# Optimization experiments

Measured on AMD Instinct MI355X. Metric: run time of the kernel, lower is better.

## Reference

```python
import math
import jax, jax.numpy as jnp
from jax import lax
import numpy as np

B, M, L = 256, 21, 512
P, S, D = 16, 8, 256
NL, EXP, H, LAM = 3, 2, 96, 0.01
T = (L - P) // S + 1  # 63 patches
HID = D * EXP


def _pos_enc():
    pe = np.zeros((T, D), np.float32)
    pos = np.arange(T, dtype=np.float32)[:, None]
    div = np.exp(np.arange(0, D, 2, dtype=np.float32) * (-math.log(10000.0) / D))
    pe[:, 0::2] = np.sin(pos * div)
    pe[:, 1::2] = np.cos(pos * div)
    return jnp.asarray(pe)


def _clin(zr, zi, Wr, Wi, br, bi):
    # faithful to torch: bias br added to both terms of yr (cancels), bi added twice in yi
    yr = (zr @ Wr.T + br) - (zi @ Wi.T + br)
    yi = (zr @ Wi.T + bi) + (zi @ Wr.T + bi)
    return yr, yi


def _softshrink(zr, zi):
    mag = jnp.sqrt(zr * zr + zi * zi)
    scale = jnp.maximum(mag - LAM, 0.0) / (mag + 1e-8) * (mag > LAM).astype(zr.dtype)
    return zr * scale, zi * scale


def _layernorm(x, g, b):
    mu = jnp.mean(x, -1, keepdims=True)
    var = jnp.mean((x - mu) ** 2, -1, keepdims=True)
    return (x - mu) / jnp.sqrt(var + 1e-5) * g + b


def _block(x, p):
    (Tw, Tb, Gew, Geb, Gpw, Gpb,
     H1Wr, H1Wi, H1br, H1bi, H2Wr, H2Wi, H2br, H2bi, lng, lnb) = p
    g = jax.nn.gelu(x @ Gew.T + Geb, approximate=False) @ Gpw.T + Gpb
    zf = jnp.fft.rfft(x, axis=1)  # FFT along time/patch axis T
    zr, zi = zf.real, zf.imag
    zr, zi = _clin(zr, zi, H1Wr, H1Wi, H1br, H1bi)
    zr, zi = _softshrink(zr, zi)
    zr, zi = _clin(zr, zi, H2Wr, H2Wi, H2br, H2bi)
    pt = jnp.fft.irfft(lax.complex(zr, zi), n=x.shape[1], axis=1)
    out = (g * pt) @ Tw.T + Tb
    return _layernorm(out + x, lng, lnb)


def _forward(x, conv_w, conv_b, tp, sp, gate_w, gate_b, proj_w, proj_b):
    # per-instance, per-variable norm over time (biased std, eps on std)
    mean = jnp.mean(x, -1, keepdims=True)
    std = jnp.sqrt(jnp.mean((x - mean) ** 2, -1, keepdims=True))
    xn = (x - mean) / (std + 1e-5)
    patches = lax.conv_general_dilated(xn, conv_w, (S,), 'VALID',
                                       dimension_numbers=('NCH', 'OIH', 'NCH'))
    patches = patches + conv_b[None, :, None]
    h = patches.transpose(0, 2, 1) + _pos_enc()[None]  # (B, T, D)
    t = h
    s = h
    for i in range(NL):
        t = _block(t, tuple(a[i] for a in tp))
        s = _block(s, tuple(a[i] for a in sp))
    gate = jax.nn.sigmoid(t @ gate_w.T + gate_b)
    feat = gate * t + (1.0 - gate) * s
    out = feat.reshape(feat.shape[0], -1) @ proj_w.T + proj_b
    y = out.reshape(-1, M, H) * (std + 1e-5) + mean
    return y


def setup_inputs() -> dict:
    key = jax.random.key(0)
    ks = iter(jax.random.split(key, 64))

    def nrm(shape, scale):
        return jax.random.normal(next(ks), shape, jnp.float32) * scale

    inp = {'x': nrm((B, M, L), 1.0)}
    inp['conv_w'] = nrm((D, M, P), 1.0 / math.sqrt(M * P))
    inp['conv_b'] = jnp.zeros((D,), jnp.float32)

    def layer_params(prefix):
        d = {}
        d[prefix + 'Tw'] = nrm((NL, D, D), 1.0 / math.sqrt(D))
        d[prefix + 'Tb'] = jnp.zeros((NL, D), jnp.float32)
        d[prefix + 'Gew'] = nrm((NL, HID, D), 1.0 / math.sqrt(D))
        d[prefix + 'Geb'] = jnp.zeros((NL, HID), jnp.float32)
        d[prefix + 'Gpw'] = nrm((NL, D, HID), 1.0 / math.sqrt(HID))
        d[prefix + 'Gpb'] = jnp.zeros((NL, D), jnp.float32)
        for hname in ('H1', 'H2'):
            d[prefix + hname + 'Wr'] = nrm((NL, D, D), 1.0 / math.sqrt(D))
            d[prefix + hname + 'Wi'] = nrm((NL, D, D), 1.0 / math.sqrt(D))
            d[prefix + hname + 'br'] = jnp.zeros((NL, D), jnp.float32)
            d[prefix + hname + 'bi'] = jnp.zeros((NL, D), jnp.float32)
        d[prefix + 'lng'] = jnp.ones((NL, D), jnp.float32)
        d[prefix + 'lnb'] = jnp.zeros((NL, D), jnp.float32)
        return d

    inp.update(layer_params('t_'))
    inp.update(layer_params('s_'))
    inp['gate_w'] = nrm((1, D), 1.0 / math.sqrt(D))
    inp['gate_b'] = jnp.zeros((1,), jnp.float32)
    inp['proj_w'] = nrm((M * H, T * D), 1.0 / math.sqrt(T * D))
    inp['proj_b'] = jnp.zeros((M * H,), jnp.float32)
    return inp


def reference(x, conv_w, conv_b,
              t_Tw, t_Tb, t_Gew, t_Geb, t_Gpw, t_Gpb,
              t_H1Wr, t_H1Wi, t_H1br, t_H1bi, t_H2Wr, t_H2Wi, t_H2br, t_H2bi, t_lng, t_lnb,
              s_Tw, s_Tb, s_Gew, s_Geb, s_Gpw, s_Gpb,
              s_H1Wr, s_H1Wi, s_H1br, s_H1bi, s_H2Wr, s_H2Wi, s_H2br, s_H2bi, s_lng, s_lnb,
              gate_w, gate_b, proj_w, proj_b):
    tp = (t_Tw, t_Tb, t_Gew, t_Geb, t_Gpw, t_Gpb,
          t_H1Wr, t_H1Wi, t_H1br, t_H1bi, t_H2Wr, t_H2Wi, t_H2br, t_H2bi, t_lng, t_lnb)
    sp = (s_Tw, s_Tb, s_Gew, s_Geb, s_Gpw, s_Gpb,
          s_H1Wr, s_H1Wi, s_H1br, s_H1bi, s_H2Wr, s_H2Wi, s_H2br, s_H2bi, s_lng, s_lnb)
    return _forward(x, conv_w, conv_b, tp, sp, gate_w, gate_b, proj_w, proj_b)
```

## Files before the change

kernel.cpp:

```cpp
#include <hip/hip_runtime.h>
#include <cstddef>
#include <cstdint>

#define B_    256
#define M_    21
#define L_    512
#define D_    256
#define T_    63
#define F_    32
#define NT_   16128
#define HID_  512
#define KCP_  352
#define H_    96
#define LAM_  0.01f
#define PZ_   14

typedef __attribute__((ext_vector_type(8))) short short8;
typedef __attribute__((ext_vector_type(4))) float f32x4;
typedef unsigned int u32;
typedef const u32 __attribute__((address_space(1)))* gas1_t;
typedef u32 __attribute__((address_space(3)))* las3_t;

__device__ __forceinline__ void async_copy16(const void* g, void* l) {
  __builtin_amdgcn_global_load_lds((gas1_t)g, (las3_t)(uintptr_t)l, 16, 0, 0);
}
__device__ __forceinline__ unsigned short f2bf(float x) {
  unsigned u = __float_as_uint(x);
  return (unsigned short)((u + 0x7FFF + ((u >> 16) & 1)) >> 16);
}
__device__ __forceinline__ float bf2f(unsigned short u) {
  return __uint_as_float(((unsigned)u) << 16);
}
__device__ __forceinline__ float gelu_exact(float v) {
  return 0.5f * v * (1.0f + erff(v * 0.70710678118654752f));
}
__device__ __forceinline__ float block_sum256(float v, float* red4) {
  #pragma unroll
  for (int off = 32; off > 0; off >>= 1) v += __shfl_down(v, off, 64);
  if ((threadIdx.x & 63) == 0) red4[threadIdx.x >> 6] = v;
  __syncthreads();
  float r = red4[0] + red4[1] + red4[2] + red4[3];
  __syncthreads();
  return r;
}
__device__ __forceinline__ float wave_sum(float v) {
  #pragma unroll
  for (int off = 1; off < 64; off <<= 1) v += __shfl_xor(v, off, 64);
  return v;
}

struct CvtEnt { const float* src; unsigned short* dst; int rows, scol, dcol, blk0; };
struct CvtArgs { CvtEnt e[19]; int nent; };
__global__ __launch_bounds__(256) void wprep_kernel(CvtArgs a) {
  int blk = blockIdx.x, e = 0;
  while (e + 1 < a.nent && a.e[e + 1].blk0 <= blk) ++e;
  CvtEnt en = a.e[e];
  int idx = (blk - en.blk0) * 256 + threadIdx.x;
  int total = en.rows * en.dcol;
  if (idx >= total) return;
  int r = idx / en.dcol, c = idx - r * en.dcol;
  float v = (c < en.scol) ? en.src[(size_t)r * en.scol + c] : 0.f;
  en.dst[idx] = f2bf(v);
}

struct CatArgs { const float* wr[12]; const float* wi[12]; };
__global__ __launch_bounds__(256) void wcat_kernel(CatArgs a, unsigned short* dst) {
  int e = blockIdx.x >> 10;
  int idx = ((blockIdx.x & 1023) << 8) + threadIdx.x;
  int r = idx >> 9, c = idx & 511;
  int cp = r >> 1, p = r & 1, d = c >> 1, q = c & 1;
  const float* wr = a.wr[e];
  const float* wi = a.wi[e];
  float v;
  if (p == 0) v = (q == 0) ? wr[cp * 256 + d] : -wi[cp * 256 + d];
  else        v = (q == 0) ? wi[cp * 256 + d] :  wr[cp * 256 + d];
  dst[(size_t)e * 262144 + idx] = f2bf(v);
}

template <int ACT, int OUTBF, int BIASM, int KSTEPS, int CVTA, int CVTW,
          int SHRINK, int MULPT, int SPLITK, int BK>
__global__ __launch_bounds__(256) void mm_kernel(
    const void* __restrict__ Av,
    const unsigned short* __restrict__ W0, const unsigned short* __restrict__ W1,
    const float* __restrict__ Wf,
    const float* __restrict__ b0, const float* __restrict__ b1,
    const unsigned short* __restrict__ ptb,
    void* __restrict__ Cv,
    const int K, const int Dout, const int ksteps_rt, const int yhalf, const int prow) {
  constexpr int NP = BK / 32;
  __shared__ __align__(16) unsigned short As[NP * 128 * 32];
  __shared__ __align__(16) unsigned short Bs[NP * 128 * 32];
  const int ksteps = KSTEPS ? KSTEPS : ksteps_rt;
  const int tid = threadIdx.x, w = tid >> 6, lane = tid & 63;
  const int quad = lane >> 4, r16 = lane & 15;
  const int kst = SPLITK ? (int)blockIdx.z * ksteps * BK : 0;
  const int tower = ((int)blockIdx.y >= yhalf) ? 1 : 0;
  const unsigned short* Wb = tower ? W1 : W0;
  const float* bias = tower ? b1 : b0;

  const unsigned short* Ab = (const unsigned short*)Av;
  const float* Af = (const float*)Av;
  const unsigned short* gA = nullptr;
  unsigned short* lA = As + (w * 32) * 32;
  if (!CVTA) gA = Ab + (size_t)(blockIdx.y * 128 + w * 32 + (lane >> 2)) * K
                     + kst + (lane & 3) * 8;
  const unsigned short* gB = nullptr;
  unsigned short* lB = Bs + (w * 32) * 32;
  if (!CVTW) gB = Wb + (size_t)(blockIdx.x * 128 + w * 32 + (lane >> 2)) * K
                     + kst + (lane & 3) * 8;
  const int crow = tid >> 3;
  const int ck4  = (tid & 7) << 2;

  f32x4 acc[4][4];
  #pragma unroll
  for (int i = 0; i < 4; ++i)
    #pragma unroll
    for (int j = 0; j < 4; ++j)
      #pragma unroll
      for (int r = 0; r < 4; ++r) acc[i][j][r] = 0.f;

  for (int ks = 0; ks < ksteps; ++ks) {
    if (!CVTA) {
      #pragma unroll
      for (int p = 0; p < NP; ++p) {
        async_copy16(gA + p * 32, lA + p * 4096);
        async_copy16(gA + (size_t)16 * K + p * 32, lA + p * 4096 + 16 * 32);
      }
      gA += BK;
    } else {
      #pragma unroll
      for (int p = 0; p < NP; ++p)
        #pragma unroll
        for (int rr = 0; rr < 4; ++rr) {
          int row128 = crow + 32 * rr;
          const float* asrc = Af + (size_t)((int)blockIdx.y * 128 + row128) * K
                                 + ks * BK + p * 32 + ck4;
          float4 v = *reinterpret_cast<const float4*>(asrc);
          ushort4 o; o.x = f2bf(v.x); o.y = f2bf(v.y); o.z = f2bf(v.z); o.w = f2bf(v.w);
          *reinterpret_cast<ushort4*>(As + p * 4096 + row128 * 32 + ck4) = o;
        }
    }
    if (!CVTW) {
      #pragma unroll
      for (int p = 0; p < NP; ++p) {
        async_copy16(gB + p * 32, lB + p * 4096);
        async_copy16(gB + (size_t)16 * K + p * 32, lB + p * 4096 + 16 * 32);
      }
      gB += BK;
    } else {
      #pragma unroll
      for (int p = 0; p < NP; ++p)
        #pragma unroll
        for (int rr = 0; rr < 4; ++rr) {
          int row128 = crow + 32 * rr;
          int wrow = blockIdx.x * 128 + row128;
          if (wrow >= Dout) wrow = Dout - 1;
          const float* wsrc = Wf + (size_t)wrow * K + kst + ks * BK + p * 32 + ck4;
          float4 v = *reinterpret_cast<const float4*>(wsrc);
          ushort4 o; o.x = f2bf(v.x); o.y = f2bf(v.y); o.z = f2bf(v.z); o.w = f2bf(v.w);
          *reinterpret_cast<ushort4*>(Bs + p * 4096 + row128 * 32 + ck4) = o;
        }
    }
    __syncthreads();
    #pragma unroll
    for (int p = 0; p < NP; ++p) {
      const unsigned short* pa = As + p * 4096 + (64 * (w >> 1) + r16) * 32 + quad * 8;
      const unsigned short* pb = Bs + p * 4096 + (64 * (w & 1) + r16) * 32 + quad * 8;
      short8 af[4], bfv[4];
      #pragma unroll
      for (int i = 0; i < 4; ++i) af[i] = *reinterpret_cast<const short8*>(pa + i * 512);
      #pragma unroll
      for (int j = 0; j < 4; ++j) bfv[j] = *reinterpret_cast<const short8*>(pb + j * 512);
      #pragma unroll
      for (int i = 0; i < 4; ++i)
        #pragma unroll
        for (int j = 0; j < 4; ++j)
          acc[i][j] = __builtin_amdgcn_mfma_f32_16x16x32_bf16(af[i], bfv[j], acc[i][j], 0, 0, 0);
    }
    __syncthreads();
  }

  float* Cf = (float*)Cv;
  unsigned short* Cb = (unsigned short*)Cv;
  if (SPLITK) Cf += (size_t)blockIdx.z * prow * Dout;
  const int colb = blockIdx.x * 128 + 64 * (w & 1) + r16;
  const int rowb = blockIdx.y * 128 + 64 * (w >> 1) + quad * 4;
  #pragma unroll
  for (int j = 0; j < 4; ++j) {
    int col = colb + 16 * j;
    float bv = 0.f;
    if (BIASM == 0) bv = bias[col];
    else if (BIASM == 1) bv = (col & 1) ? 2.0f * bias[col >> 1] : 0.f;
    bool colok = (BIASM != 2) || (col < Dout);
    #pragma unroll
    for (int i = 0; i < 4; ++i) {
      #pragma unroll
      for (int r = 0; r < 4; ++r) {
        int row = rowb + 16 * i + r;
        float v = acc[i][j][r] + bv;
        if (ACT == 1) v = gelu_exact(v);
        if (SHRINK) {
          float o = __shfl_xor(v, 1, 64);
          float mag = sqrtf(v * v + o * o);
          float s = (mag > LAM_) ? (mag - LAM_) / (mag + 1e-8f) : 0.f;
          v *= s;
        }
        if (MULPT) v *= bf2f(ptb[(size_t)row * Dout + col]);
        if (colok) {
          if (OUTBF) Cb[(size_t)row * Dout + col] = f2bf(v);
          else       Cf[(size_t)row * Dout + col] = v;
        }
      }
    }
  }
}

__global__ __launch_bounds__(256) void norm_kernel(const float* __restrict__ x,
    float* __restrict__ xn, float* __restrict__ meanb, float* __restrict__ stdb) {
  __shared__ float red[4];
  int bm = blockIdx.x;
  const float* xr = x + (size_t)bm * L_;
  float v0 = xr[threadIdx.x], v1 = xr[threadIdx.x + 256];
  float mu = block_sum256(v0 + v1, red) * (1.0f / L_);
  float d0 = v0 - mu, d1 = v1 - mu;
  float sd = sqrtf(block_sum256(d0 * d0 + d1 * d1, red) * (1.0f / L_));
  float inv = 1.0f / (sd + 1e-5f);
  float* xo = xn + (size_t)bm * L_;
  xo[threadIdx.x] = d0 * inv;
  xo[threadIdx.x + 256] = d1 * inv;
  if (threadIdx.x == 0) { meanb[bm] = mu; stdb[bm] = sd; }
}

__global__ __launch_bounds__(256) void im2col_kernel(const float* __restrict__ xn,
                                                     unsigned short* __restrict__ im) {
  int row = blockIdx.x;
  int b = row / T_, t = row - b * T_;
  const float* xb = xn + (size_t)b * M_ * L_ + t * 8;
  unsigned short* o = im + (size_t)row * KCP_;
  for (int i = threadIdx.x; i < KCP_; i += 256) {
    float v = 0.f;
    if (i < 336) { int m = i >> 4, p = i & 15; v = xb[m * L_ + p]; }
    o[i] = f2bf(v);
  }
}

__global__ __launch_bounds__(256) void add_pe_kernel(const float* __restrict__ g0,
                                                     float* __restrict__ x32) {
  int row = blockIdx.x, d = threadIdx.x;
  int t = row % T_;
  size_t idx = (size_t)row * D_ + d;
  float freq = expf((float)(d & ~1) * (-9.210340371976184f / 256.0f));
  float ang = (float)t * freq;
  float pe = (d & 1) ? cosf(ang) : sinf(ang);
  float h = g0[idx] + pe;
  x32[idx] = h;
  x32[idx + (size_t)NT_ * D_] = h;
}

__global__ __launch_bounds__(256) void dft_kernel(const float* __restrict__ X,
                                                  unsigned short* __restrict__ Zcat) {
  __shared__ float2 tw[T_ * F_];
  int bt = blockIdx.x, d = threadIdx.x;
  for (int i = threadIdx.x; i < T_ * F_; i += 256) {
    int t = i >> 5, f = i & 31;
    int k = (f * t) % T_;
    float sn, cs;
    sincosf((6.283185307179586f / 63.0f) * (float)k, &sn, &cs);
    tw[i] = make_float2(cs, -sn);
  }
  __syncthreads();
  const float* xb = X + (size_t)bt * T_ * D_ + d;
  float ar[F_], ai[F_];
  #pragma unroll
  for (int f = 0; f < F_; ++f) { ar[f] = 0.f; ai[f] = 0.f; }
  for (int t = 0; t < T_; ++t) {
    float v = xb[(size_t)t * D_];
    const float2* w = &tw[t * F_];
    #pragma unroll
    for (int f = 0; f < F_; ++f) {
      float2 c = w[f];
      ar[f] = fmaf(v, c.x, ar[f]);
      ai[f] = fmaf(v, c.y, ai[f]);
    }
  }
  u32* z = reinterpret_cast<u32*>(Zcat + (size_t)bt * F_ * 512);
  #pragma unroll
  for (int f = 0; f < F_; ++f)
    z[f * 256 + d] = (u32)f2bf(ar[f]) | ((u32)f2bf(ai[f]) << 16);
}

__global__ __launch_bounds__(256) void irfft_kernel(const unsigned short* __restrict__ Y,
                                                    unsigned short* __restrict__ ptb) {
  __shared__ float2 tw[T_ * 31];
  int bt = blockIdx.x, d = threadIdx.x;
  for (int i = threadIdx.x; i < T_ * 31; i += 256) {
    int t = i / 31, f = i - t * 31 + 1;
    int k = (f * t) % T_;
    float sn, cs;
    sincosf((6.283185307179586f / 63.0f) * (float)k, &sn, &cs);
    tw[i] = make_float2(cs * (2.0f / 63.0f), -sn * (2.0f / 63.0f));
  }
  __syncthreads();
  const unsigned short* yb = Y + (size_t)bt * F_ * 512 + 2 * d;
  float y0 = bf2f(yb[0]) * (1.0f / 63.0f);
  float yr[31], yi[31];
  #pragma unroll
  for (int f = 1; f < F_; ++f) {
    u32 p = *reinterpret_cast<const u32*>(yb + (size_t)f * 512);
    yr[f - 1] = bf2f((unsigned short)(p & 0xffff));
    yi[f - 1] = bf2f((unsigned short)(p >> 16));
  }
  unsigned short* po = ptb + (size_t)bt * T_ * D_ + d;
  for (int t = 0; t < T_; ++t) {
    const float2* w = &tw[t * 31];
    float acc0 = y0, acc1 = 0.f;
    #pragma unroll
    for (int f = 0; f < 31; f += 2) {
      float2 c = w[f];
      acc0 = fmaf(yr[f], c.x, fmaf(yi[f], c.y, acc0));
      if (f + 1 < 31) {
        float2 c1 = w[f + 1];
        acc1 = fmaf(yr[f + 1], c1.x, fmaf(yi[f + 1], c1.y, acc1));
      }
    }
    po[(size_t)t * D_] = f2bf(acc0 + acc1);
  }
}

__global__ __launch_bounds__(256) void ln_kernel(const float* __restrict__ outb,
    float* __restrict__ x, const float* __restrict__ g0, const float* __restrict__ b0,
    const float* __restrict__ g1, const float* __restrict__ b1, int yhalf) {
  int row = blockIdx.x * 4 + (threadIdx.x >> 6);
  int lane = threadIdx.x & 63;
  const float* g = (row >= yhalf) ? g1 : g0;
  const float* b = (row >= yhalf) ? b1 : b0;
  size_t base = (size_t)row * D_ + lane * 4;
  float4 ov = *reinterpret_cast<const float4*>(outb + base);
  float4 xv = *reinterpret_cast<const float4*>(x + base);
  float v0 = ov.x + xv.x, v1 = ov.y + xv.y, v2 = ov.z + xv.z, v3 = ov.w + xv.w;
  float mu = wave_sum(v0 + v1 + v2 + v3) * (1.0f / D_);
  v0 -= mu; v1 -= mu; v2 -= mu; v3 -= mu;
  float var = wave_sum(v0 * v0 + v1 * v1 + v2 * v2 + v3 * v3) * (1.0f / D_);
  float is = rsqrtf(var + 1e-5f);
  float4 gv = *reinterpret_cast<const float4*>(g + lane * 4);
  float4 bv = *reinterpret_cast<const float4*>(b + lane * 4);
  float4 o;
  o.x = v0 * is * gv.x + bv.x;
  o.y = v1 * is * gv.y + bv.y;
  o.z = v2 * is * gv.z + bv.z;
  o.w = v3 * is * gv.w + bv.w;
  *reinterpret_cast<float4*>(x + base) = o;
}

__global__ __launch_bounds__(256) void gate_feat_kernel(const float* __restrict__ x32,
    const float* __restrict__ gw, const float* __restrict__ gb,
    unsigned short* __restrict__ featbf) {
  int row = blockIdx.x * 4 + (threadIdx.x >> 6);
  int lane = threadIdx.x & 63;
  size_t base = (size_t)row * D_ + lane * 4;
  float4 tv = *reinterpret_cast<const float4*>(x32 + base);
  float4 sv = *reinterpret_cast<const float4*>(x32 + base + (size_t)NT_ * D_);
  float4 gv = *reinterpret_cast<const float4*>(gw + lane * 4);
  float dot = wave_sum(tv.x * gv.x + tv.y * gv.y + tv.z * gv.z + tv.w * gv.w) + gb[0];
  float gate = 1.0f / (1.0f + expf(-dot));
  ushort4 o;
  o.x = f2bf(gate * tv.x + (1.0f - gate) * sv.x);
  o.y = f2bf(gate * tv.y + (1.0f - gate) * sv.y);
  o.z = f2bf(gate * tv.z + (1.0f - gate) * sv.z);
  o.w = f2bf(gate * tv.w + (1.0f - gate) * sv.w);
  *reinterpret_cast<ushort4*>(featbf + base) = o;
}

__global__ __launch_bounds__(256) void final_kernel(const float* __restrict__ part,
    const float* __restrict__ pb, const float* __restrict__ stdb,
    const float* __restrict__ meanb, float* __restrict__ y) {
  int i = blockIdx.x * 256 + threadIdx.x;
  float acc = 0.f;
  #pragma unroll
  for (int z = 0; z < PZ_; ++z) acc += part[(size_t)z * 516096 + i];
  int b = i / 2016;
  int col = i - b * 2016;
  int m = col / H_;
  float sc = stdb[b * M_ + m] + 1e-5f;
  y[i] = (acc + pb[col]) * sc + meanb[b * M_ + m];
}

extern "C" void kernel_launch(void* const* d_in, const int* in_sizes, int n_in,
                              void* d_out, int out_size, void* d_ws, size_t ws_size,
                              hipStream_t stream) {
  const float* x      = (const float*)d_in[0];
  const float* conv_w = (const float*)d_in[1];
  const float* conv_b = (const float*)d_in[2];
  const float* tP[16];
  const float* sP[16];
  for (int i = 0; i < 16; ++i) tP[i] = (const float*)d_in[3 + i];
  for (int i = 0; i < 16; ++i) sP[i] = (const float*)d_in[19 + i];
  const float* gate_w = (const float*)d_in[35];
  const float* gate_b = (const float*)d_in[36];
  const float* proj_w = (const float*)d_in[37];
  const float* proj_b = (const float*)d_in[38];
  float* out = (float*)d_out;

  float* ws    = (float*)d_ws;
  float* x32   = ws;
  unsigned short* wb = (unsigned short*)(x32 + 8257536);
  float* meanb = x32 + 8257536 + 2600960;
  float* stdb  = meanb + 5376;
  float* R1    = stdb + 5376 + 16;
  float* R2    = R1 + 8388608;

  unsigned short* im2colB = (unsigned short*)R1;
  unsigned short* Zcat    = (unsigned short*)R1;
  unsigned short* Ycat1   = (unsigned short*)(R1 + 4194304);
  unsigned short* ptb     = (unsigned short*)(R1 + 4194304);
  unsigned short* gp      = (unsigned short*)R1;
  unsigned short* featbf  = (unsigned short*)R1;

  float* xn     = R2;
  float* g0buf  = R2;
  unsigned short* Ycat2b = (unsigned short*)R2;
  unsigned short* hidB = (unsigned short*)R2;
  float* outb   = R2;
  float* part   = R2;

  unsigned short* convW = wb;
  unsigned short* sets  = wb + 90112;
  unsigned short* catW  = wb + 90112 + 1966080;

  CvtArgs ca; int blk0 = 0, ne = 0;
  auto add_ent = [&](const float* s, unsigned short* d, int rows, int scol, int dcol) {
    ca.e[ne].src = s; ca.e[ne].dst = d; ca.e[ne].rows = rows;
    ca.e[ne].scol = scol; ca.e[ne].dcol = dcol; ca.e[ne].blk0 = blk0;
    blk0 += (rows * dcol + 255) / 256; ++ne;
  };
  add_ent(conv_w, convW, 256, 336, 352);
  for (int tw = 0; tw < 2; ++tw) {
    const float** Pp = tw ? (const float**)sP : (const float**)tP;
    for (int l = 0; l < 3; ++l) {
      unsigned short* sb = sets + (size_t)(tw * 3 + l) * 327680;
      add_ent(Pp[2] + (size_t)l * 131072, sb,          512, 256, 256);
      add_ent(Pp[4] + (size_t)l * 131072, sb + 131072, 256, 512, 512);
      add_ent(Pp[0] + (size_t)l * 65536,  sb + 262144, 256, 256, 256);
    }
  }
  ca.nent = ne;
  wprep_kernel<<<blk0, 256, 0, stream>>>(ca);

  CatArgs cat;
  for (int tw = 0; tw < 2; ++tw) {
    const float** Pp = tw ? (const float**)sP : (const float**)tP;
    for (int l = 0; l < 3; ++l) {
      int e0 = (tw * 3 + l) * 2;
      cat.wr[e0]     = Pp[6]  + (size_t)l * 65536;
      cat.wi[e0]     = Pp[7]  + (size_t)l * 65536;
      cat.wr[e0 + 1] = Pp[10] + (size_t)l * 65536;
      cat.wi[e0 + 1] = Pp[11] + (size_t)l * 65536;
    }
  }
  wcat_kernel<<<12 * 1024, 256, 0, stream>>>(cat, catW);

  norm_kernel<<<B_ * M_, 256, 0, stream>>>(x, xn, meanb, stdb);
  im2col_kernel<<<NT_, 256, 0, stream>>>(xn, im2colB);
  mm_kernel<0, 0, 0, 11, 0, 0, 0, 0, 0, 32><<<dim3(2, 126), 256, 0, stream>>>(
      im2colB, convW, convW, nullptr, conv_b, conv_b, nullptr, g0buf,
      KCP_, 256, 0, 1 << 30, 0);
  add_pe_kernel<<<NT_, 256, 0, stream>>>(g0buf, x32);

  for (int l = 0; l < 3; ++l) {
    unsigned short* st0 = sets + (size_t)l * 327680;
    unsigned short* st1 = sets + (size_t)(3 + l) * 327680;
    unsigned short* c1t0 = catW + (size_t)((0 + l) * 2) * 262144;
    unsigned short* c2t0 = c1t0 + 262144;
    unsigned short* c1t1 = catW + (size_t)((3 + l) * 2) * 262144;
    unsigned short* c2t1 = c1t1 + 262144;

    dft_kernel<<<2 * B_, 256, 0, stream>>>(x32, Zcat);
    mm_kernel<0, 1, 1, 8, 0, 0, 1, 0, 0, 64><<<dim3(4, 128), 256, 0, stream>>>(
        Zcat, c1t0, c1t1, nullptr, tP[9] + (size_t)l * D_, sP[9] + (size_t)l * D_,
        nullptr, Ycat1, 512, 512, 0, 64, 0);
    mm_kernel<0, 1, 1, 8, 0, 0, 0, 0, 0, 64><<<dim3(4, 128), 256, 0, stream>>>(
        Ycat1, c2t0, c2t1, nullptr, tP[13] + (size_t)l * D_, sP[13] + (size_t)l * D_,
        nullptr, Ycat2b, 512, 512, 0, 64, 0);
    irfft_kernel<<<2 * B_, 256, 0, stream>>>(Ycat2b, ptb);
    mm_kernel<1, 1, 0, 4, 1, 0, 0, 0, 0, 64><<<dim3(4, 252), 256, 0, stream>>>(
        x32, st0, st1, nullptr, tP[3] + (size_t)l * HID_, sP[3] + (size_t)l * HID_,
        nullptr, hidB, 256, 512, 0, 126, 0);
    mm_kernel<0, 1, 0, 8, 0, 0, 0, 1, 0, 64><<<dim3(2, 252), 256, 0, stream>>>(
        hidB, st0 + 131072, st1 + 131072, nullptr,
        tP[5] + (size_t)l * D_, sP[5] + (size_t)l * D_, ptb, gp, 512, 256, 0, 126, 0);
    mm_kernel<0, 0, 0, 4, 0, 0, 0, 0, 0, 64><<<dim3(2, 252), 256, 0, stream>>>(
        gp, st0 + 262144, st1 + 262144, nullptr,
        tP[1] + (size_t)l * D_, sP[1] + (size_t)l * D_, nullptr, outb, 256, 256, 0, 126, 0);
    ln_kernel<<<2 * NT_ / 4, 256, 0, stream>>>(outb, x32,
        tP[14] + (size_t)l * D_, tP[15] + (size_t)l * D_,
        sP[14] + (size_t)l * D_, sP[15] + (size_t)l * D_, NT_);
  }

  gate_feat_kernel<<<NT_ / 4, 256, 0, stream>>>(x32, gate_w, gate_b, featbf);
  mm_kernel<0, 0, 2, 0, 0, 1, 0, 0, 1, 32><<<dim3(16, 2, PZ_), 256, 0, stream>>>(
      featbf, nullptr, nullptr, proj_w, nullptr, nullptr, nullptr, part,
      NT_, 2016, 504 / PZ_, 1 << 30, 256);
  final_kernel<<<2016, 256, 0, stream>>>(part, proj_b, stdb, meanb, out);
}
```

Measured before the change: 1.022 ms.

## Halve GEMM row tile via RT template, prefetch fp32 operands into registers

Adds an RT template parameter so every GEMM uses 64-row A tiles instead of 128, doubling grid size in y for all matmul launches to raise occupancy and block count. Fp32-converted A and W tiles are now loaded into registers one k-step ahead, overlapping global loads with MFMA work. The split-K projection is retiled to 16 partitions with a clamped tail. Smaller tiles lower per-block reuse of the B tile and increase total weight traffic.

```diff
diff --git a/kernel.cpp b/kernel.cpp
--- a/kernel.cpp
+++ b/kernel.cpp
@@ -13,7 +13,7 @@
 #define KCP_  352
 #define H_    96
 #define LAM_  0.01f
-#define PZ_   14
+#define PZ_   16
 
 typedef __attribute__((ext_vector_type(8))) short short8;
 typedef __attribute__((ext_vector_type(4))) float f32x4;
@@ -78,7 +78,7 @@
 }
 
 template <int ACT, int OUTBF, int BIASM, int KSTEPS, int CVTA, int CVTW,
-          int SHRINK, int MULPT, int SPLITK, int BK>
+          int SHRINK, int MULPT, int SPLITK, int BK, int RT>
 __global__ __launch_bounds__(256) void mm_kernel(
     const void* __restrict__ Av,
     const unsigned short* __restrict__ W0, const unsigned short* __restrict__ W1,
@@ -86,14 +86,18 @@
     const float* __restrict__ b0, const float* __restrict__ b1,
     const unsigned short* __restrict__ ptb,
     void* __restrict__ Cv,
-    const int K, const int Dout, const int ksteps_rt, const int yhalf, const int prow) {
+    const int K, const int Dout, const int ksteps_rt, const int yhalf,
+    const int prow, const int totk) {
   constexpr int NP = BK / 32;
-  __shared__ __align__(16) unsigned short As[NP * 128 * 32];
+  constexpr int RWS = 32 * RT;
+  __shared__ __align__(16) unsigned short As[NP * RWS * 32];
   __shared__ __align__(16) unsigned short Bs[NP * 128 * 32];
-  const int ksteps = KSTEPS ? KSTEPS : ksteps_rt;
   const int tid = threadIdx.x, w = tid >> 6, lane = tid & 63;
   const int quad = lane >> 4, r16 = lane & 15;
-  const int kst = SPLITK ? (int)blockIdx.z * ksteps * BK : 0;
+  int nks = KSTEPS ? KSTEPS : ksteps_rt;
+  const int ksbeg = SPLITK ? (int)blockIdx.z * nks : 0;
+  if (SPLITK) { int rem = totk - ksbeg; if (nks > rem) nks = rem; }
+  const int kst = ksbeg * BK;
   const int tower = ((int)blockIdx.y >= yhalf) ? 1 : 0;
   const unsigned short* Wb = tower ? W1 : W0;
   const float* bias = tower ? b1 : b0;
@@ -101,43 +105,66 @@
   const unsigned short* Ab = (const unsigned short*)Av;
   const float* Af = (const float*)Av;
   const unsigned short* gA = nullptr;
-  unsigned short* lA = As + (w * 32) * 32;
-  if (!CVTA) gA = Ab + (size_t)(blockIdx.y * 128 + w * 32 + (lane >> 2)) * K
+  unsigned short* lA = As + (w * 8 * RT) * 32;
+  if (!CVTA) gA = Ab + (size_t)((int)blockIdx.y * RWS + w * 8 * RT + (lane >> 2)) * K
                      + kst + (lane & 3) * 8;
   const unsigned short* gB = nullptr;
   unsigned short* lB = Bs + (w * 32) * 32;
-  if (!CVTW) gB = Wb + (size_t)(blockIdx.x * 128 + w * 32 + (lane >> 2)) * K
+  if (!CVTW) gB = Wb + (size_t)((int)blockIdx.x * 128 + w * 32 + (lane >> 2)) * K
                      + kst + (lane & 3) * 8;
   const int crow = tid >> 3;
   const int ck4  = (tid & 7) << 2;
 
-  f32x4 acc[4][4];
-  #pragma unroll
-  for (int i = 0; i < 4; ++i)
+  float4 areg[NP][RT];
+  float4 wreg[NP][4];
+  auto loadA = [&](int ksi) {
+    #pragma unroll
+    for (int p = 0; p < NP; ++p)
+      #pragma unroll
+      for (int rr = 0; rr < RT; ++rr)
+        areg[p][rr] = *reinterpret_cast<const float4*>(
+            Af + (size_t)((int)blockIdx.y * RWS + crow + 32 * rr) * K
+               + kst + ksi * BK + p * 32 + ck4);
+  };
+  auto loadW = [&](int ksi) {
+    #pragma unroll
+    for (int p = 0; p < NP; ++p)
+      #pragma unroll
+      for (int rr = 0; rr < 4; ++rr) {
+        int wrow = (int)blockIdx.x * 128 + crow + 32 * rr;
+        if (wrow >= Dout) wrow = Dout - 1;
+        wreg[p][rr] = *reinterpret_cast<const float4*>(
+            Wf + (size_t)wrow * K + kst + ksi * BK + p * 32 + ck4);
+      }
+  };
+  if (CVTA) loadA(0);
+  if (CVTW) loadW(0);
+
+  f32x4 acc[RT][4];
+  #pragma unroll
+  for (int i = 0; i < RT; ++i)
     #pragma unroll
     for (int j = 0; j < 4; ++j)
       #pragma unroll
       for (int r = 0; r < 4; ++r) acc[i][j][r] = 0.f;
 
-  for (int ks = 0; ks < ksteps; ++ks) {
+  for (int ks = 0; ks < nks; ++ks) {
     if (!CVTA) {
       #pragma unroll
-      for (int p = 0; p < NP; ++p) {
-        async_copy16(gA + p * 32, lA + p * 4096);
-        async_copy16(gA + (size_t)16 * K + p * 32, lA + p * 4096 + 16 * 32);
-      }
+      for (int p = 0; p < NP; ++p)
+        #pragma unroll
+        for (int c = 0; c < RT / 2; ++c)
+          async_copy16(gA + (size_t)(c * 16) * K + p * 32,
+                       lA + p * (RWS * 32) + c * 16 * 32);
       gA += BK;
     } else {
       #pragma unroll
       for (int p = 0; p < NP; ++p)
         #pragma unroll
-        for (int rr = 0; rr < 4; ++rr) {
-          int row128 = crow + 32 * rr;
-          const float* asrc = Af + (size_t)((int)blockIdx.y * 128 + row128) * K
-                                 + ks * BK + p * 32 + ck4;
-          float4 v = *reinterpret_cast<const float4*>(asrc);
+        for (int rr = 0; rr < RT; ++rr) {
+          float4 v = areg[p][rr];
           ushort4 o; o.x = f2bf(v.x); o.y = f2bf(v.y); o.z = f2bf(v.z); o.w = f2bf(v.w);
-          *reinterpret_cast<ushort4*>(As + p * 4096 + row128 * 32 + ck4) = o;
+          *reinterpret_cast<ushort4*>(As + p * (RWS * 32) + (crow + 32 * rr) * 32 + ck4) = o;
         }
     }
     if (!CVTW) {
@@ -152,27 +179,25 @@
       for (int p = 0; p < NP; ++p)
         #pragma unroll
         for (int rr = 0; rr < 4; ++rr) {
-          int row128 = crow + 32 * rr;
-          int wrow = blockIdx.x * 128 + row128;
-          if (wrow >= Dout) wrow = Dout - 1;
-          const float* wsrc = Wf + (size_t)wrow * K + kst + ks * BK + p * 32 + ck4;
-          float4 v = *reinterpret_cast<const float4*>(wsrc);
+          float4 v = wreg[p][rr];
           ushort4 o; o.x = f2bf(v.x); o.y = f2bf(v.y); o.z = f2bf(v.z); o.w = f2bf(v.w);
-          *reinterpret_cast<ushort4*>(Bs + p * 4096 + row128 * 32 + ck4) = o;
+          *reinterpret_cast<ushort4*>(Bs + p * 4096 + (crow + 32 * rr) * 32 + ck4) = o;
         }
     }
     __syncthreads();
+    if (CVTA && ks + 1 < nks) loadA(ks + 1);
+    if (CVTW && ks + 1 < nks) loadW(ks + 1);
     #pragma unroll
     for (int p = 0; p < NP; ++p) {
-      const unsigned short* pa = As + p * 4096 + (64 * (w >> 1) + r16) * 32 + quad * 8;
+      const unsigned short* pa = As + p * (RWS * 32) + ((w >> 1) * 16 * RT + r16) * 32 + quad * 8;
       const unsigned short* pb = Bs + p * 4096 + (64 * (w & 1) + r16) * 32 + quad * 8;
-      short8 af[4], bfv[4];
-      #pragma unroll
-      for (int i = 0; i < 4; ++i) af[i] = *reinterpret_cast<const short8*>(pa + i * 512);
+      short8 af[RT], bfv[4];
+      #pragma unroll
+      for (int i = 0; i < RT; ++i) af[i] = *reinterpret_cast<const short8*>(pa + i * 512);
       #pragma unroll
       for (int j = 0; j < 4; ++j) bfv[j] = *reinterpret_cast<const short8*>(pb + j * 512);
       #pragma unroll
-      for (int i = 0; i < 4; ++i)
+      for (int i = 0; i < RT; ++i)
         #pragma unroll
         for (int j = 0; j < 4; ++j)
           acc[i][j] = __builtin_amdgcn_mfma_f32_16x16x32_bf16(af[i], bfv[j], acc[i][j], 0, 0, 0);
@@ -183,8 +208,8 @@
   float* Cf = (float*)Cv;
   unsigned short* Cb = (unsigned short*)Cv;
   if (SPLITK) Cf += (size_t)blockIdx.z * prow * Dout;
-  const int colb = blockIdx.x * 128 + 64 * (w & 1) + r16;
-  const int rowb = blockIdx.y * 128 + 64 * (w >> 1) + quad * 4;
+  const int colb = (int)blockIdx.x * 128 + 64 * (w & 1) + r16;
+  const int rowb = (int)blockIdx.y * RWS + 16 * RT * (w >> 1) + quad * 4;
   #pragma unroll
   for (int j = 0; j < 4; ++j) {
     int col = colb + 16 * j;
@@ -193,7 +218,7 @@
     else if (BIASM == 1) bv = (col & 1) ? 2.0f * bias[col >> 1] : 0.f;
     bool colok = (BIASM != 2) || (col < Dout);
     #pragma unroll
-    for (int i = 0; i < 4; ++i) {
+    for (int i = 0; i < RT; ++i) {
       #pragma unroll
       for (int r = 0; r < 4; ++r) {
         int row = rowb + 16 * i + r;
@@ -461,9 +486,9 @@
 
   norm_kernel<<<B_ * M_, 256, 0, stream>>>(x, xn, meanb, stdb);
   im2col_kernel<<<NT_, 256, 0, stream>>>(xn, im2colB);
-  mm_kernel<0, 0, 0, 11, 0, 0, 0, 0, 0, 32><<<dim3(2, 126), 256, 0, stream>>>(
+  mm_kernel<0, 0, 0, 11, 0, 0, 0, 0, 0, 32, 2><<<dim3(2, 252), 256, 0, stream>>>(
       im2colB, convW, convW, nullptr, conv_b, conv_b, nullptr, g0buf,
-      KCP_, 256, 0, 1 << 30, 0);
+      KCP_, 256, 0, 1 << 30, 0, 0);
   add_pe_kernel<<<NT_, 256, 0, stream>>>(g0buf, x32);
 
   for (int l = 0; l < 3; ++l) {
@@ -475,30 +500,30 @@
     unsigned short* c2t1 = c1t1 + 262144;
 
     dft_kernel<<<2 * B_, 256, 0, stream>>>(x32, Zcat);
-    mm_kernel<0, 1, 1, 8, 0, 0, 1, 0, 0, 64><<<dim3(4, 128), 256, 0, stream>>>(
+    mm_kernel<0, 1, 1, 8, 0, 0, 1, 0, 0, 64, 2><<<dim3(4, 256), 256, 0, stream>>>(
         Zcat, c1t0, c1t1, nullptr, tP[9] + (size_t)l * D_, sP[9] + (size_t)l * D_,
-        nullptr, Ycat1, 512, 512, 0, 64, 0);
-    mm_kernel<0, 1, 1, 8, 0, 0, 0, 0, 0, 64><<<dim3(4, 128), 256, 0, stream>>>(
+        nullptr, Ycat1, 512, 512, 0, 128, 0, 0);
+    mm_kernel<0, 1, 1, 8, 0, 0, 0, 0, 0, 64, 2><<<dim3(4, 256), 256, 0, stream>>>(
         Ycat1, c2t0, c2t1, nullptr, tP[13] + (size_t)l * D_, sP[13] + (size_t)l * D_,
-        nullptr, Ycat2b, 512, 512, 0, 64, 0);
+        nullptr, Ycat2b, 512, 512, 0, 128, 0, 0);
     irfft_kernel<<<2 * B_, 256, 0, stream>>>(Ycat2b, ptb);
-    mm_kernel<1, 1, 0, 4, 1, 0, 0, 0, 0, 64><<<dim3(4, 252), 256, 0, stream>>>(
+    mm_kernel<1, 1, 0, 4, 1, 0, 0, 0, 0, 64, 2><<<dim3(4, 504), 256, 0, stream>>>(
         x32, st0, st1, nullptr, tP[3] + (size_t)l * HID_, sP[3] + (size_t)l * HID_,
-        nullptr, hidB, 256, 512, 0, 126, 0);
-    mm_kernel<0, 1, 0, 8, 0, 0, 0, 1, 0, 64><<<dim3(2, 252), 256, 0, stream>>>(
+        nullptr, hidB, 256, 512, 0, 252, 0, 0);
+    mm_kernel<0, 1, 0, 8, 0, 0, 0, 1, 0, 64, 2><<<dim3(2, 504), 256, 0, stream>>>(
         hidB, st0 + 131072, st1 + 131072, nullptr,
-        tP[5] + (size_t)l * D_, sP[5] + (size_t)l * D_, ptb, gp, 512, 256, 0, 126, 0);
-    mm_kernel<0, 0, 0, 4, 0, 0, 0, 0, 0, 64><<<dim3(2, 252), 256, 0, stream>>>(
+        tP[5] + (size_t)l * D_, sP[5] + (size_t)l * D_, ptb, gp, 512, 256, 0, 252, 0, 0);
+    mm_kernel<0, 0, 0, 4, 0, 0, 0, 0, 0, 64, 2><<<dim3(2, 504), 256, 0, stream>>>(
         gp, st0 + 262144, st1 + 262144, nullptr,
-        tP[1] + (size_t)l * D_, sP[1] + (size_t)l * D_, nullptr, outb, 256, 256, 0, 126, 0);
+        tP[1] + (size_t)l * D_, sP[1] + (size_t)l * D_, nullptr, outb, 256, 256, 0, 252, 0, 0);
     ln_kernel<<<2 * NT_ / 4, 256, 0, stream>>>(outb, x32,
         tP[14] + (size_t)l * D_, tP[15] + (size_t)l * D_,
         sP[14] + (size_t)l * D_, sP[15] + (size_t)l * D_, NT_);
   }
 
   gate_feat_kernel<<<NT_ / 4, 256, 0, stream>>>(x32, gate_w, gate_b, featbf);
-  mm_kernel<0, 0, 2, 0, 0, 1, 0, 0, 1, 32><<<dim3(16, 2, PZ_), 256, 0, stream>>>(
+  mm_kernel<0, 0, 2, 0, 0, 1, 0, 0, 1, 32, 2><<<dim3(16, 4, PZ_), 256, 0, stream>>>(
       featbf, nullptr, nullptr, proj_w, nullptr, nullptr, nullptr, part,
-      NT_, 2016, 504 / PZ_, 1 << 30, 256);
+      NT_, 2016, 32, 1 << 30, 256, 504);
   final_kernel<<<2016, 256, 0, stream>>>(part, proj_b, stdb, meanb, out);
 }
```

After: 1.010 ms. No clear change (-1.3%).
